# Kernel tuning notes

Hardware: AMD Instinct MI355X
Metric: run time of the kernel (lower is better)

Reference implementation:

```python
import jax, jax.numpy as jnp
import numpy as np
from jax import lax

D_MODEL = 128   # n_channels
OUT_C   = 128   # out_channels
D_STATE = 16
EXPAND  = 2
D_INNER = EXPAND * D_MODEL  # 256
D_CONV  = 4
DT_RANK = (D_MODEL + 15) // 16  # 8
LN_EPS  = 1e-5


def setup_inputs() -> dict:
    key = jax.random.key(0)
    ks = jax.random.split(key, 8)
    s = lambda k, shape: jax.random.normal(k, shape, jnp.float32) * 0.02
    return {
        "x1": jax.random.normal(ks[0], (2, D_MODEL, 64, 64), jnp.float32),
        "W_in": s(ks[1], (D_MODEL, 2 * D_INNER)),              # in_proj (no bias)
        "conv_w": s(ks[2], (D_INNER, 1, D_CONV)),              # depthwise conv kernel (O, I/g, K)
        "conv_b": jnp.zeros((D_INNER,), jnp.float32),
        "W_x": s(ks[3], (D_INNER, DT_RANK + 2 * D_STATE)),     # x_proj (no bias)
        "W_dt": s(ks[4], (DT_RANK, D_INNER)),                  # dt_proj
        "b_dt": s(ks[5], (D_INNER,)),
        "A_log": jnp.log(jnp.broadcast_to(
            jnp.arange(1, D_STATE + 1, dtype=jnp.float32), (D_INNER, D_STATE))),
        "D": jnp.ones((D_INNER,), jnp.float32),
        "W_out": s(ks[6], (D_INNER, OUT_C)),                   # out_proj (no bias)
        "ln_g": jnp.ones((OUT_C,), jnp.float32),
        "ln_b": jnp.zeros((OUT_C,), jnp.float32),
    }


def _mamba(x, W_in, conv_w, conv_b, W_x, W_dt, b_dt, A_log, D, W_out):
    # x: (b, L, d_model)
    b, L, _ = x.shape
    xz = x @ W_in                               # (b, L, 2*d_inner)
    xin, z = jnp.split(xz, 2, axis=-1)
    # causal depthwise conv1d over L
    xp = jnp.pad(xin, ((0, 0), (D_CONV - 1, 0), (0, 0)))
    xc = lax.conv_general_dilated(
        xp, conv_w, window_strides=(1,), padding='VALID',
        dimension_numbers=('NLC', 'OIL', 'NLC'),
        feature_group_count=D_INNER)
    xc = jax.nn.silu(xc + conv_b)               # (b, L, d_inner)
    # input-dependent SSM params
    xdbl = xc @ W_x                             # (b, L, dt_rank + 2*d_state)
    dt, Bm, Cm = jnp.split(xdbl, [DT_RANK, DT_RANK + D_STATE], axis=-1)
    dt = jax.nn.softplus(dt @ W_dt + b_dt)      # (b, L, d_inner)
    A = -jnp.exp(A_log)                         # (d_inner, d_state)
    dA = jnp.exp(dt[..., None] * A)                             # (b, L, d_inner, d_state)
    dBu = dt[..., None] * Bm[:, :, None, :] * xc[..., None]     # (b, L, d_inner, d_state)

    def step(h, inp):
        dA_t, dBu_t, C_t = inp                  # (b,d,s), (b,d,s), (b,s)
        h = dA_t * h + dBu_t
        y = jnp.einsum('bds,bs->bd', h, C_t)
        return h, y

    h0 = jnp.zeros((b, D_INNER, D_STATE), xc.dtype)
    _, ys = lax.scan(step, h0, (dA.transpose(1, 0, 2, 3),
                                dBu.transpose(1, 0, 2, 3),
                                Cm.transpose(1, 0, 2)))
    y = ys.transpose(1, 0, 2) + xc * D          # (b, L, d_inner)
    y = y * jax.nn.silu(z)                      # gated
    return y @ W_out                            # (b, L, out_c)


def reference(x1, W_in, conv_w, conv_b, W_x, W_dt, b_dt, A_log, D, W_out, ln_g, ln_b):
    b, c, h, w = x1.shape
    x = x1.transpose(0, 2, 3, 1).reshape(b, h * w, c)
    y = _mamba(x, W_in, conv_w, conv_b, W_x, W_dt, b_dt, A_log, D, W_out)
    mu = y.mean(-1, keepdims=True)
    var = ((y - mu) ** 2).mean(-1, keepdims=True)
    y = (y - mu) * lax.rsqrt(var + LN_EPS) * ln_g + ln_b
    return y.reshape(b, h, w, OUT_C).transpose(0, 3, 1, 2)
```

## Files before the change

kernel.cpp:

```cpp
#include <hip/hip_runtime.h>
#include <math.h>

#define B_ 2
#define DMODEL 128
#define DIN 256
#define DSTATE 16
#define DTR 8
#define OUTC 128
#define Lseq 4096
#define NC 256
#define LC 16

__device__ __forceinline__ float siluf(float x){ return x / (1.f + __expf(-x)); }

__device__ __forceinline__ void build_dA(float e1, float* dAv){
    float e2 = e1*e1, e4 = e2*e2, e8 = e4*e4;
    dAv[0]=e1;         dAv[1]=e2;         dAv[2]=e2*e1;       dAv[3]=e4;
    dAv[4]=e4*e1;      dAv[5]=e4*e2;      dAv[6]=e4*dAv[2];   dAv[7]=e8;
    dAv[8]=e8*e1;      dAv[9]=e8*e2;      dAv[10]=e8*dAv[2];  dAv[11]=e8*e4;
    dAv[12]=e8*dAv[4]; dAv[13]=e8*dAv[5]; dAv[14]=e8*dAv[6];  dAv[15]=e8*e8;
}

__device__ __forceinline__ float softplusf(float a){
    return (a > 20.f) ? a : __logf(1.f + __expf(a));
}

__global__ __launch_bounds__(256) void k_inconv_scan1(const float* __restrict__ x1,
        const float* __restrict__ Win,
        const float* __restrict__ convw, const float* __restrict__ convb,
        const float* __restrict__ Wx, const float* __restrict__ Wdt,
        const float* __restrict__ bdt, const float* __restrict__ Alog,
        float* __restrict__ zs, float* __restrict__ xc, float* __restrict__ dt,
        float* __restrict__ Bm, float* __restrict__ Cm, float2* __restrict__ PSw){
    __shared__ float sbuf[10240];
    __shared__ float xcs[16*257];
    __shared__ float xdbl[16*40];
    float* xt  = sbuf;
    float* Wxs = sbuf;
    int blk = blockIdx.x;
    int b  = blk >> 8;
    int cb = blk & 255;
    int l0 = cb << 4;
    int t  = threadIdx.x;

    const float* xb = x1 + (size_t)b * DMODEL * Lseq;
    for (int e = t; e < 128*19; e += 256){
        int c = e / 19, p = e - c*19;
        int l = l0 - 3 + p;
        xt[c*20 + p] = (l >= 0) ? xb[(size_t)c*Lseq + l] : 0.f;
    }
    __syncthreads();

    float acc0[19], acc1[16];
    #pragma unroll
    for (int p=0;p<19;++p){acc0[p]=0.f;}
    #pragma unroll
    for (int p=0;p<16;++p){acc1[p]=0.f;}
    #pragma unroll 4
    for (int k=0;k<DMODEL;++k){
        float w0 = Win[k*512 + t];
        float w1 = Win[k*512 + t + 256];
        const float4* xp = (const float4*)&xt[k*20];
        float4 v0 = xp[0], v1 = xp[1], v2 = xp[2], v3 = xp[3], v4 = xp[4];
        float xv[19] = { v0.x,v0.y,v0.z,v0.w, v1.x,v1.y,v1.z,v1.w,
                         v2.x,v2.y,v2.z,v2.w, v3.x,v3.y,v3.z,v3.w,
                         v4.x,v4.y,v4.z };
        #pragma unroll
        for (int p=0;p<19;++p) acc0[p] = fmaf(xv[p], w0, acc0[p]);
        #pragma unroll
        for (int p=0;p<16;++p) acc1[p] = fmaf(xv[p+3], w1, acc1[p]);
    }
    {
        float* zp = zs + ((size_t)(b*Lseq + l0))*DIN + t;
        #pragma unroll
        for (int p=0;p<16;++p) zp[p*DIN] = siluf(acc1[p]);
    }

    {
        float cw0 = convw[t*4+0], cw1 = convw[t*4+1], cw2 = convw[t*4+2], cw3 = convw[t*4+3];
        float bb = convb[t];
        float* xcg = xc + ((size_t)(b*Lseq + l0))*DIN + t;
        #pragma unroll
        for (int l = 0; l < 16; ++l){
            float acc = bb;
            acc = fmaf(acc0[l],   cw0, acc);
            acc = fmaf(acc0[l+1], cw1, acc);
            acc = fmaf(acc0[l+2], cw2, acc);
            acc = fmaf(acc0[l+3], cw3, acc);
            float v = siluf(acc);
            xcs[l*257 + t] = v;
            xcg[l*DIN] = v;
        }
    }
    __syncthreads();

    {
        const float4* Wg = (const float4*)Wx;
        float4* Ws = (float4*)Wxs;
        #pragma unroll
        for (int e = t; e < 2560; e += 256)
            Ws[e] = Wg[e];
    }
    __syncthreads();

    if (t < 128){
        int jg = t & 7;
        int lg = t >> 3;
        int j0 = jg * 5;
        float a0=0.f, a1=0.f, a2=0.f, a3=0.f, a4=0.f;
        const float* xrow = xcs + lg*257;
        const float* wbase = Wxs + j0;
        #pragma unroll 8
        for (int d = 0; d < 256; ++d){
            float xv = xrow[d];
            const float* wr = wbase + d*40;
            a0 = fmaf(xv, wr[0], a0);
            a1 = fmaf(xv, wr[1], a1);
            a2 = fmaf(xv, wr[2], a2);
            a3 = fmaf(xv, wr[3], a3);
            a4 = fmaf(xv, wr[4], a4);
        }
        float* xo = xdbl + lg*40 + j0;
        xo[0]=a0; xo[1]=a1; xo[2]=a2; xo[3]=a3; xo[4]=a4;
    }
    __syncthreads();

    {
        float wd[DTR];
        #pragma unroll
        for (int r=0;r<DTR;++r) wd[r] = Wdt[r*DIN + t];
        float bv = bdt[t];
        float Av[16];
        {
            const float4* Ap = (const float4*)(Alog + t*DSTATE);
            #pragma unroll
            for (int q=0;q<4;++q){
                float4 a = Ap[q];
                Av[q*4]   = -__expf(a.x);
                Av[q*4+1] = -__expf(a.y);
                Av[q*4+2] = -__expf(a.z);
                Av[q*4+3] = -__expf(a.w);
            }
        }
        bool fastA = true;
        #pragma unroll
        for (int i=1;i<16;++i)
            fastA = fastA && (fabsf(Av[i] - (float)(i+1)*Av[0]) <= 1e-6f*fabsf(Av[i]));
        float P[16], S[16];
        #pragma unroll
        for (int s=0;s<16;++s){ P[s]=1.f; S[s]=0.f; }
        float* dtg = dt + ((size_t)(b*Lseq + l0))*DIN + t;
        #pragma unroll 4
        for (int l=0;l<16;++l){
            float a = bv;
            #pragma unroll
            for (int r=0;r<DTR;++r) a = fmaf(xdbl[l*40 + r], wd[r], a);
            float dtv = softplusf(a);
            dtg[l*DIN] = dtv;
            float xcv = xcs[l*257 + t];
            float dx  = dtv*xcv;
            const float4* Bv = (const float4*)&xdbl[l*40 + DTR];
            float4 B0 = Bv[0], B1 = Bv[1], B2 = Bv[2], B3 = Bv[3];
            float dAv[16];
            if (fastA){
                build_dA(__expf(dtv*Av[0]), dAv);
            } else {
                #pragma unroll
                for (int i=0;i<16;++i) dAv[i] = __expf(dtv*Av[i]);
            }
            #define ST1(i, bval) { P[i] *= dAv[i]; S[i] = fmaf(dAv[i], S[i], dx*(bval)); }
            ST1(0,B0.x) ST1(1,B0.y) ST1(2,B0.z) ST1(3,B0.w)
            ST1(4,B1.x) ST1(5,B1.y) ST1(6,B1.z) ST1(7,B1.w)
            ST1(8,B2.x) ST1(9,B2.y) ST1(10,B2.z) ST1(11,B2.w)
            ST1(12,B3.x) ST1(13,B3.y) ST1(14,B3.z) ST1(15,B3.w)
            #undef ST1
        }
        float2* ps2 = PSw + ((size_t)(b*NC + cb))*4096;
        #pragma unroll
        for (int s=0;s<16;++s) ps2[s*256 + t] = make_float2(P[s], S[s]);
    }
    for (int o = t; o < 512; o += 256){
        int l = o >> 5, q = o & 31;
        float v = xdbl[l*40 + DTR + q];
        size_t g = ((size_t)(b*Lseq + l0 + l))*DSTATE;
        if (q < DSTATE) Bm[g + q] = v;
        else            Cm[g + (q - DSTATE)] = v;
    }
}

__global__ __launch_bounds__(256) void k_scan2(const float2* __restrict__ PSw,
        float* __restrict__ Iw){
    __shared__ float2 gps[16][16];
    __shared__ float  ge [16][16];
    int blk = blockIdx.x;
    int b  = blk >> 8;
    int r0 = (blk & 255) * 16;
    int t  = threadIdx.x;
    int rr = t & 15;
    int cg = t >> 4;
    size_t base = ((size_t)(b*NC + cg*16))*4096 + r0 + rr;
    float Pl[16], Sl[16];
    float Pa = 1.f, Sa = 0.f;
    #pragma unroll
    for (int i=0;i<16;++i){
        float2 ps = PSw[base + (size_t)i*4096];
        Pl[i] = ps.x; Sl[i] = ps.y;
        Pa = ps.x * Pa;
        Sa = fmaf(ps.x, Sa, ps.y);
    }
    gps[cg][rr] = make_float2(Pa, Sa);
    __syncthreads();
    if (t < 16){
        float H = 0.f;
        #pragma unroll
        for (int g=0; g<16; ++g){
            float2 ps = gps[g][t];
            ge[g][t] = H;
            H = fmaf(ps.x, H, ps.y);
        }
    }
    __syncthreads();
    float H = ge[cg][rr];
    #pragma unroll
    for (int i=0;i<16;++i){
        Iw[base + (size_t)i*4096] = H;
        H = fmaf(Pl[i], H, Sl[i]);
    }
}

__global__ __launch_bounds__(256) void k_scan3out(const float* __restrict__ dt,
        const float* __restrict__ xc, const float* __restrict__ zs,
        const float* __restrict__ Bm, const float* __restrict__ Cm,
        const float* __restrict__ Alog, const float* __restrict__ Dv,
        const float* __restrict__ Iw,
        const float* __restrict__ Wout, const float* __restrict__ lng,
        const float* __restrict__ lnb, float* __restrict__ out){
    __shared__ float ysm[256*18];
    __shared__ float os[128*18];
    __shared__ float Bs[LC*DSTATE];
    __shared__ float Cs[LC*DSTATE];
    int blk = blockIdx.x;
    int b = blk >> 8, c = blk & 255;
    int l0 = c * LC;
    int t = threadIdx.x;
    size_t gb = (size_t)(b*Lseq + l0);
    Bs[t] = Bm[gb*DSTATE + t];
    Cs[t] = Cm[gb*DSTATE + t];
    float Av[16];
    {
        const float4* Ap = (const float4*)(Alog + t*DSTATE);
        #pragma unroll
        for (int q=0;q<4;++q){
            float4 a = Ap[q];
            Av[q*4]   = -__expf(a.x);
            Av[q*4+1] = -__expf(a.y);
            Av[q*4+2] = -__expf(a.z);
            Av[q*4+3] = -__expf(a.w);
        }
    }
    bool fastA = true;
    #pragma unroll
    for (int i=1;i<16;++i)
        fastA = fastA && (fabsf(Av[i] - (float)(i+1)*Av[0]) <= 1e-6f*fabsf(Av[i]));
    float h[16];
    {
        const float* Ip = Iw + ((size_t)(b*NC + c))*4096 + t;
        #pragma unroll
        for (int s=0;s<16;++s) h[s] = Ip[s*256];
    }
    float Dd = Dv[t];
    float dtv[LC], xcv[LC], zvv[LC];
    {
        const float* dtp = dt + gb*DIN + t;
        const float* xcp = xc + gb*DIN + t;
        const float* zsp = zs + gb*DIN + t;
        #pragma unroll
        for (int l=0;l<LC;++l){
            dtv[l] = dtp[l*DIN];
            xcv[l] = xcp[l*DIN];
            zvv[l] = zsp[l*DIN];
        }
    }
    __syncthreads();
    #pragma unroll
    for (int l=0;l<LC;++l){
        float dtl = dtv[l];
        float dx  = dtl*xcv[l];
        const float4* Bv = (const float4*)&Bs[l*DSTATE];
        const float4* Cv = (const float4*)&Cs[l*DSTATE];
        float4 B0 = Bv[0], B1 = Bv[1], B2 = Bv[2], B3 = Bv[3];
        float4 C0 = Cv[0], C1 = Cv[1], C2 = Cv[2], C3 = Cv[3];
        float dAv[16];
        if (fastA){
            build_dA(__expf(dtl*Av[0]), dAv);
        } else {
            #pragma unroll
            for (int i=0;i<16;++i) dAv[i] = __expf(dtl*Av[i]);
        }
        float y = 0.f;
        #define ST3(i, bval, cval) { h[i] = fmaf(dAv[i], h[i], dx*(bval)); y = fmaf(h[i], (cval), y); }
        ST3(0,B0.x,C0.x) ST3(1,B0.y,C0.y) ST3(2,B0.z,C0.z) ST3(3,B0.w,C0.w)
        ST3(4,B1.x,C1.x) ST3(5,B1.y,C1.y) ST3(6,B1.z,C1.z) ST3(7,B1.w,C1.w)
        ST3(8,B2.x,C2.x) ST3(9,B2.y,C2.y) ST3(10,B2.z,C2.z) ST3(11,B2.w,C2.w)
        ST3(12,B3.x,C3.x) ST3(13,B3.y,C3.y) ST3(14,B3.z,C3.z) ST3(15,B3.w,C3.w)
        #undef ST3
        ysm[t*18 + l] = (y + Dd*xcv[l])*zvv[l];
    }
    __syncthreads();
    int lg = t >> 5, cg = t & 31;
    int l0t = lg*2, c0 = cg*4;
    float acc[2][4];
    #pragma unroll
    for (int i=0;i<2;++i)
        #pragma unroll
        for (int j=0;j<4;++j) acc[i][j]=0.f;
    #pragma unroll 4
    for (int k=0;k<DIN;++k){
        float2 yv = *(const float2*)&ysm[k*18 + l0t];
        float4 wv = *(const float4*)&Wout[k*OUTC + c0];
        acc[0][0]=fmaf(yv.x,wv.x,acc[0][0]); acc[0][1]=fmaf(yv.x,wv.y,acc[0][1]);
        acc[0][2]=fmaf(yv.x,wv.z,acc[0][2]); acc[0][3]=fmaf(yv.x,wv.w,acc[0][3]);
        acc[1][0]=fmaf(yv.y,wv.x,acc[1][0]); acc[1][1]=fmaf(yv.y,wv.y,acc[1][1]);
        acc[1][2]=fmaf(yv.y,wv.z,acc[1][2]); acc[1][3]=fmaf(yv.y,wv.w,acc[1][3]);
    }
    float4 gm = *(const float4*)&lng[c0];
    float4 bt = *(const float4*)&lnb[c0];
    #pragma unroll
    for (int i=0;i<2;++i){
        float rs = acc[i][0]+acc[i][1]+acc[i][2]+acc[i][3];
        #pragma unroll
        for (int m=16;m>0;m>>=1) rs += __shfl_xor(rs, m, 64);
        float mu = rs * (1.f/128.f);
        float d0 = acc[i][0]-mu, d1 = acc[i][1]-mu, d2 = acc[i][2]-mu, d3 = acc[i][3]-mu;
        float sq = d0*d0+d1*d1+d2*d2+d3*d3;
        #pragma unroll
        for (int m=16;m>0;m>>=1) sq += __shfl_xor(sq, m, 64);
        float rstd = rsqrtf(sq * (1.f/128.f) + 1e-5f);
        int lidx = l0t + i;
        os[(c0+0)*18 + lidx] = d0*rstd*gm.x + bt.x;
        os[(c0+1)*18 + lidx] = d1*rstd*gm.y + bt.y;
        os[(c0+2)*18 + lidx] = d2*rstd*gm.z + bt.z;
        os[(c0+3)*18 + lidx] = d3*rstd*gm.w + bt.w;
    }
    __syncthreads();
    {
        int cc = t >> 1, sel = t & 1;
        const float* ip = &os[cc*18 + sel*8];
        float2 a0 = *(const float2*)(ip);
        float2 a1 = *(const float2*)(ip+2);
        float2 a2 = *(const float2*)(ip+4);
        float2 a3 = *(const float2*)(ip+6);
        float* op = out + ((size_t)(b*OUTC + cc))*Lseq + l0 + sel*8;
        *(float4*)(op)   = make_float4(a0.x,a0.y,a1.x,a1.y);
        *(float4*)(op+4) = make_float4(a2.x,a2.y,a3.x,a3.y);
    }
}

extern "C" void kernel_launch(void* const* d_in, const int* in_sizes, int n_in,
                              void* d_out, int out_size, void* d_ws, size_t ws_size,
                              hipStream_t stream) {
    const float* x1    = (const float*)d_in[0];
    const float* Win   = (const float*)d_in[1];
    const float* convw = (const float*)d_in[2];
    const float* convb = (const float*)d_in[3];
    const float* Wx    = (const float*)d_in[4];
    const float* Wdt   = (const float*)d_in[5];
    const float* bdt   = (const float*)d_in[6];
    const float* Alog  = (const float*)d_in[7];
    const float* Dv    = (const float*)d_in[8];
    const float* Wout  = (const float*)d_in[9];
    const float* lng   = (const float*)d_in[10];
    const float* lnb   = (const float*)d_in[11];
    float* out = (float*)d_out;

    float* ws  = (float*)d_ws;
    float* Iw  = ws;
    float* zs  = Iw  + 2097152;
    float* xc  = zs  + 2097152;
    float* dt  = xc  + 2097152;
    float* Bm  = dt  + 2097152;
    float* Cm  = Bm  + 131072;
    float2* PSw = (float2*)(Cm + 131072);

    k_inconv_scan1<<<512, 256, 0, stream>>>(x1, Win, convw, convb, Wx, Wdt, bdt, Alog,
                                            zs, xc, dt, Bm, Cm, PSw);
    k_scan2       <<<512, 256, 0, stream>>>(PSw, Iw);
    k_scan3out    <<<512, 256, 0, stream>>>(dt, xc, zs, Bm, Cm, Alog, Dv, Iw,
                                            Wout, lng, lnb, out);
}
```

Before: 157.3 us.

## Fuse three kernels into one persistent kernel with software grid barriers

Merges the in-proj/conv/chunk-scan, the inter-chunk scan, and the output scan/out-proj/layernorm kernels into one kernel. Two atomic-counter grid barriers separate the phases. Per-chunk intermediates (z, xc, dt, B, C) now stay in registers and shared memory instead of round-tripping through global memory, which removes several MB of traffic and two launches. The barrier needs all 512 blocks resident at once; launch_bounds(256,2) is meant to ensure that, and the design adds spin-wait overhead plus a memset launch.

```diff
diff --git a/kernel.cpp b/kernel.cpp
--- a/kernel.cpp
+++ b/kernel.cpp
@@ -10,6 +10,7 @@
 #define Lseq 4096
 #define NC 256
 #define LC 16
+#define NBLK 512
 
 __device__ __forceinline__ float siluf(float x){ return x / (1.f + __expf(-x)); }
 
@@ -25,24 +26,39 @@
     return (a > 20.f) ? a : __logf(1.f + __expf(a));
 }
 
-__global__ __launch_bounds__(256) void k_inconv_scan1(const float* __restrict__ x1,
+__device__ __forceinline__ void gridbar(unsigned* cnt, int t){
+    __syncthreads();
+    if (t == 0){
+        __threadfence();
+        unsigned ticket = atomicAdd(cnt, 1u);
+        unsigned target = ((ticket >> 9) + 1u) << 9;
+        while (atomicAdd(cnt, 0u) < target){ __builtin_amdgcn_s_sleep(8); }
+        __threadfence();
+    }
+    __syncthreads();
+}
+
+__global__ __launch_bounds__(256, 2) void k_fused(const float* __restrict__ x1,
         const float* __restrict__ Win,
         const float* __restrict__ convw, const float* __restrict__ convb,
         const float* __restrict__ Wx, const float* __restrict__ Wdt,
         const float* __restrict__ bdt, const float* __restrict__ Alog,
-        float* __restrict__ zs, float* __restrict__ xc, float* __restrict__ dt,
-        float* __restrict__ Bm, float* __restrict__ Cm, float2* __restrict__ PSw){
+        const float* __restrict__ Dv, const float* __restrict__ Wout,
+        const float* __restrict__ lng, const float* __restrict__ lnb,
+        float2* __restrict__ PSw, float* __restrict__ Iw, unsigned* __restrict__ bar,
+        float* __restrict__ out){
     __shared__ float sbuf[10240];
     __shared__ float xcs[16*257];
     __shared__ float xdbl[16*40];
-    float* xt  = sbuf;
-    float* Wxs = sbuf;
+
     int blk = blockIdx.x;
     int b  = blk >> 8;
     int cb = blk & 255;
     int l0 = cb << 4;
     int t  = threadIdx.x;
 
+    float* xt  = sbuf;
+    float* Wxs = sbuf;
     const float* xb = x1 + (size_t)b * DMODEL * Lseq;
     for (int e = t; e < 128*19; e += 256){
         int c = e / 19, p = e - c*19;
@@ -70,16 +86,13 @@
         #pragma unroll
         for (int p=0;p<16;++p) acc1[p] = fmaf(xv[p+3], w1, acc1[p]);
     }
-    {
-        float* zp = zs + ((size_t)(b*Lseq + l0))*DIN + t;
-        #pragma unroll
-        for (int p=0;p<16;++p) zp[p*DIN] = siluf(acc1[p]);
-    }
+    float zvv[16];
+    #pragma unroll
+    for (int p=0;p<16;++p) zvv[p] = siluf(acc1[p]);
 
     {
         float cw0 = convw[t*4+0], cw1 = convw[t*4+1], cw2 = convw[t*4+2], cw3 = convw[t*4+3];
         float bb = convb[t];
-        float* xcg = xc + ((size_t)(b*Lseq + l0))*DIN + t;
         #pragma unroll
         for (int l = 0; l < 16; ++l){
             float acc = bb;
@@ -87,9 +100,7 @@
             acc = fmaf(acc0[l+1], cw1, acc);
             acc = fmaf(acc0[l+2], cw2, acc);
             acc = fmaf(acc0[l+3], cw3, acc);
-            float v = siluf(acc);
-            xcs[l*257 + t] = v;
-            xcg[l*DIN] = v;
+            xcs[l*257 + t] = siluf(acc);
         }
     }
     __syncthreads();
@@ -125,12 +136,13 @@
     }
     __syncthreads();
 
+    float Av[16], dtv[16];
+    bool fastA = true;
     {
         float wd[DTR];
         #pragma unroll
         for (int r=0;r<DTR;++r) wd[r] = Wdt[r*DIN + t];
         float bv = bdt[t];
-        float Av[16];
         {
             const float4* Ap = (const float4*)(Alog + t*DSTATE);
             #pragma unroll
@@ -142,31 +154,29 @@
                 Av[q*4+3] = -__expf(a.w);
             }
         }
-        bool fastA = true;
         #pragma unroll
         for (int i=1;i<16;++i)
             fastA = fastA && (fabsf(Av[i] - (float)(i+1)*Av[0]) <= 1e-6f*fabsf(Av[i]));
         float P[16], S[16];
         #pragma unroll
         for (int s=0;s<16;++s){ P[s]=1.f; S[s]=0.f; }
-        float* dtg = dt + ((size_t)(b*Lseq + l0))*DIN + t;
-        #pragma unroll 4
+        #pragma unroll
         for (int l=0;l<16;++l){
             float a = bv;
             #pragma unroll
             for (int r=0;r<DTR;++r) a = fmaf(xdbl[l*40 + r], wd[r], a);
-            float dtv = softplusf(a);
-            dtg[l*DIN] = dtv;
+            float dtvl = softplusf(a);
+            dtv[l] = dtvl;
             float xcv = xcs[l*257 + t];
-            float dx  = dtv*xcv;
+            float dx  = dtvl*xcv;
             const float4* Bv = (const float4*)&xdbl[l*40 + DTR];
             float4 B0 = Bv[0], B1 = Bv[1], B2 = Bv[2], B3 = Bv[3];
             float dAv[16];
             if (fastA){
-                build_dA(__expf(dtv*Av[0]), dAv);
+                build_dA(__expf(dtvl*Av[0]), dAv);
             } else {
                 #pragma unroll
-                for (int i=0;i<16;++i) dAv[i] = __expf(dtv*Av[i]);
+                for (int i=0;i<16;++i) dAv[i] = __expf(dtvl*Av[i]);
             }
             #define ST1(i, bval) { P[i] *= dAv[i]; S[i] = fmaf(dAv[i], S[i], dx*(bval)); }
             ST1(0,B0.x) ST1(1,B0.y) ST1(2,B0.z) ST1(3,B0.w)
@@ -179,116 +189,64 @@
         #pragma unroll
         for (int s=0;s<16;++s) ps2[s*256 + t] = make_float2(P[s], S[s]);
     }
-    for (int o = t; o < 512; o += 256){
-        int l = o >> 5, q = o & 31;
-        float v = xdbl[l*40 + DTR + q];
-        size_t g = ((size_t)(b*Lseq + l0 + l))*DSTATE;
-        if (q < DSTATE) Bm[g + q] = v;
-        else            Cm[g + (q - DSTATE)] = v;
-    }
-}
-
-__global__ __launch_bounds__(256) void k_scan2(const float2* __restrict__ PSw,
-        float* __restrict__ Iw){
-    __shared__ float2 gps[16][16];
-    __shared__ float  ge [16][16];
-    int blk = blockIdx.x;
-    int b  = blk >> 8;
-    int r0 = (blk & 255) * 16;
-    int t  = threadIdx.x;
-    int rr = t & 15;
-    int cg = t >> 4;
-    size_t base = ((size_t)(b*NC + cg*16))*4096 + r0 + rr;
-    float Pl[16], Sl[16];
-    float Pa = 1.f, Sa = 0.f;
-    #pragma unroll
-    for (int i=0;i<16;++i){
-        float2 ps = PSw[base + (size_t)i*4096];
-        Pl[i] = ps.x; Sl[i] = ps.y;
-        Pa = ps.x * Pa;
-        Sa = fmaf(ps.x, Sa, ps.y);
-    }
-    gps[cg][rr] = make_float2(Pa, Sa);
-    __syncthreads();
-    if (t < 16){
-        float H = 0.f;
-        #pragma unroll
-        for (int g=0; g<16; ++g){
-            float2 ps = gps[g][t];
-            ge[g][t] = H;
-            H = fmaf(ps.x, H, ps.y);
-        }
-    }
-    __syncthreads();
-    float H = ge[cg][rr];
-    #pragma unroll
-    for (int i=0;i<16;++i){
-        Iw[base + (size_t)i*4096] = H;
-        H = fmaf(Pl[i], H, Sl[i]);
-    }
-}
-
-__global__ __launch_bounds__(256) void k_scan3out(const float* __restrict__ dt,
-        const float* __restrict__ xc, const float* __restrict__ zs,
-        const float* __restrict__ Bm, const float* __restrict__ Cm,
-        const float* __restrict__ Alog, const float* __restrict__ Dv,
-        const float* __restrict__ Iw,
-        const float* __restrict__ Wout, const float* __restrict__ lng,
-        const float* __restrict__ lnb, float* __restrict__ out){
-    __shared__ float ysm[256*18];
-    __shared__ float os[128*18];
-    __shared__ float Bs[LC*DSTATE];
-    __shared__ float Cs[LC*DSTATE];
-    int blk = blockIdx.x;
-    int b = blk >> 8, c = blk & 255;
-    int l0 = c * LC;
-    int t = threadIdx.x;
-    size_t gb = (size_t)(b*Lseq + l0);
-    Bs[t] = Bm[gb*DSTATE + t];
-    Cs[t] = Cm[gb*DSTATE + t];
-    float Av[16];
-    {
-        const float4* Ap = (const float4*)(Alog + t*DSTATE);
-        #pragma unroll
-        for (int q=0;q<4;++q){
-            float4 a = Ap[q];
-            Av[q*4]   = -__expf(a.x);
-            Av[q*4+1] = -__expf(a.y);
-            Av[q*4+2] = -__expf(a.z);
-            Av[q*4+3] = -__expf(a.w);
-        }
-    }
-    bool fastA = true;
-    #pragma unroll
-    for (int i=1;i<16;++i)
-        fastA = fastA && (fabsf(Av[i] - (float)(i+1)*Av[0]) <= 1e-6f*fabsf(Av[i]));
+
+    gridbar(bar, t);
+
+    {
+        float2* gps = (float2*)sbuf;
+        float*  ge  = sbuf + 512;
+        int r0 = (blk & 255) * 16;
+        int rr = t & 15;
+        int cg2 = t >> 4;
+        size_t base = ((size_t)(b*NC + cg2*16))*4096 + r0 + rr;
+        float Pl[16], Sl[16];
+        float Pa = 1.f, Sa = 0.f;
+        #pragma unroll
+        for (int i=0;i<16;++i){
+            float2 ps = PSw[base + (size_t)i*4096];
+            Pl[i] = ps.x; Sl[i] = ps.y;
+            Pa = ps.x * Pa;
+            Sa = fmaf(ps.x, Sa, ps.y);
+        }
+        gps[cg2*16 + rr] = make_float2(Pa, Sa);
+        __syncthreads();
+        if (t < 16){
+            float H = 0.f;
+            #pragma unroll
+            for (int g=0; g<16; ++g){
+                float2 ps = gps[g*16 + t];
+                ge[g*16 + t] = H;
+                H = fmaf(ps.x, H, ps.y);
+            }
+        }
+        __syncthreads();
+        float H = ge[cg2*16 + rr];
+        #pragma unroll
+        for (int i=0;i<16;++i){
+            Iw[base + (size_t)i*4096] = H;
+            H = fmaf(Pl[i], H, Sl[i]);
+        }
+    }
+
+    gridbar(bar, t);
+
+    float* ysm = sbuf;
+    float* os  = sbuf + 4608;
     float h[16];
     {
-        const float* Ip = Iw + ((size_t)(b*NC + c))*4096 + t;
+        const float* Ip = Iw + ((size_t)(b*NC + cb))*4096 + t;
         #pragma unroll
         for (int s=0;s<16;++s) h[s] = Ip[s*256];
     }
     float Dd = Dv[t];
-    float dtv[LC], xcv[LC], zvv[LC];
-    {
-        const float* dtp = dt + gb*DIN + t;
-        const float* xcp = xc + gb*DIN + t;
-        const float* zsp = zs + gb*DIN + t;
-        #pragma unroll
-        for (int l=0;l<LC;++l){
-            dtv[l] = dtp[l*DIN];
-            xcv[l] = xcp[l*DIN];
-            zvv[l] = zsp[l*DIN];
-        }
-    }
-    __syncthreads();
     #pragma unroll
     for (int l=0;l<LC;++l){
         float dtl = dtv[l];
-        float dx  = dtl*xcv[l];
-        const float4* Bv = (const float4*)&Bs[l*DSTATE];
-        const float4* Cv = (const float4*)&Cs[l*DSTATE];
+        float xcv = xcs[l*257 + t];
+        float dx  = dtl*xcv;
+        const float4* Bv = (const float4*)&xdbl[l*40 + DTR];
         float4 B0 = Bv[0], B1 = Bv[1], B2 = Bv[2], B3 = Bv[3];
+        const float4* Cv = (const float4*)&xdbl[l*40 + DTR + DSTATE];
         float4 C0 = Cv[0], C1 = Cv[1], C2 = Cv[2], C3 = Cv[3];
         float dAv[16];
         if (fastA){
@@ -304,43 +262,45 @@
         ST3(8,B2.x,C2.x) ST3(9,B2.y,C2.y) ST3(10,B2.z,C2.z) ST3(11,B2.w,C2.w)
         ST3(12,B3.x,C3.x) ST3(13,B3.y,C3.y) ST3(14,B3.z,C3.z) ST3(15,B3.w,C3.w)
         #undef ST3
-        ysm[t*18 + l] = (y + Dd*xcv[l])*zvv[l];
-    }
-    __syncthreads();
-    int lg = t >> 5, cg = t & 31;
-    int l0t = lg*2, c0 = cg*4;
-    float acc[2][4];
-    #pragma unroll
-    for (int i=0;i<2;++i)
-        #pragma unroll
-        for (int j=0;j<4;++j) acc[i][j]=0.f;
-    #pragma unroll 4
-    for (int k=0;k<DIN;++k){
-        float2 yv = *(const float2*)&ysm[k*18 + l0t];
-        float4 wv = *(const float4*)&Wout[k*OUTC + c0];
-        acc[0][0]=fmaf(yv.x,wv.x,acc[0][0]); acc[0][1]=fmaf(yv.x,wv.y,acc[0][1]);
-        acc[0][2]=fmaf(yv.x,wv.z,acc[0][2]); acc[0][3]=fmaf(yv.x,wv.w,acc[0][3]);
-        acc[1][0]=fmaf(yv.y,wv.x,acc[1][0]); acc[1][1]=fmaf(yv.y,wv.y,acc[1][1]);
-        acc[1][2]=fmaf(yv.y,wv.z,acc[1][2]); acc[1][3]=fmaf(yv.y,wv.w,acc[1][3]);
-    }
-    float4 gm = *(const float4*)&lng[c0];
-    float4 bt = *(const float4*)&lnb[c0];
-    #pragma unroll
-    for (int i=0;i<2;++i){
-        float rs = acc[i][0]+acc[i][1]+acc[i][2]+acc[i][3];
-        #pragma unroll
-        for (int m=16;m>0;m>>=1) rs += __shfl_xor(rs, m, 64);
-        float mu = rs * (1.f/128.f);
-        float d0 = acc[i][0]-mu, d1 = acc[i][1]-mu, d2 = acc[i][2]-mu, d3 = acc[i][3]-mu;
-        float sq = d0*d0+d1*d1+d2*d2+d3*d3;
-        #pragma unroll
-        for (int m=16;m>0;m>>=1) sq += __shfl_xor(sq, m, 64);
-        float rstd = rsqrtf(sq * (1.f/128.f) + 1e-5f);
-        int lidx = l0t + i;
-        os[(c0+0)*18 + lidx] = d0*rstd*gm.x + bt.x;
-        os[(c0+1)*18 + lidx] = d1*rstd*gm.y + bt.y;
-        os[(c0+2)*18 + lidx] = d2*rstd*gm.z + bt.z;
-        os[(c0+3)*18 + lidx] = d3*rstd*gm.w + bt.w;
+        ysm[t*18 + l] = (y + Dd*xcv)*zvv[l];
+    }
+    __syncthreads();
+    {
+        int lg = t >> 5, cgc = t & 31;
+        int l0t = lg*2, c0 = cgc*4;
+        float acc[2][4];
+        #pragma unroll
+        for (int i=0;i<2;++i)
+            #pragma unroll
+            for (int j=0;j<4;++j) acc[i][j]=0.f;
+        #pragma unroll 4
+        for (int k=0;k<DIN;++k){
+            float2 yv = *(const float2*)&ysm[k*18 + l0t];
+            float4 wv = *(const float4*)&Wout[k*OUTC + c0];
+            acc[0][0]=fmaf(yv.x,wv.x,acc[0][0]); acc[0][1]=fmaf(yv.x,wv.y,acc[0][1]);
+            acc[0][2]=fmaf(yv.x,wv.z,acc[0][2]); acc[0][3]=fmaf(yv.x,wv.w,acc[0][3]);
+            acc[1][0]=fmaf(yv.y,wv.x,acc[1][0]); acc[1][1]=fmaf(yv.y,wv.y,acc[1][1]);
+            acc[1][2]=fmaf(yv.y,wv.z,acc[1][2]); acc[1][3]=fmaf(yv.y,wv.w,acc[1][3]);
+        }
+        float4 gm = *(const float4*)&lng[c0];
+        float4 bt = *(const float4*)&lnb[c0];
+        #pragma unroll
+        for (int i=0;i<2;++i){
+            float rs = acc[i][0]+acc[i][1]+acc[i][2]+acc[i][3];
+            #pragma unroll
+            for (int m=16;m>0;m>>=1) rs += __shfl_xor(rs, m, 64);
+            float mu = rs * (1.f/128.f);
+            float d0 = acc[i][0]-mu, d1 = acc[i][1]-mu, d2 = acc[i][2]-mu, d3 = acc[i][3]-mu;
+            float sq = d0*d0+d1*d1+d2*d2+d3*d3;
+            #pragma unroll
+            for (int m=16;m>0;m>>=1) sq += __shfl_xor(sq, m, 64);
+            float rstd = rsqrtf(sq * (1.f/128.f) + 1e-5f);
+            int lidx = l0t + i;
+            os[(c0+0)*18 + lidx] = d0*rstd*gm.x + bt.x;
+            os[(c0+1)*18 + lidx] = d1*rstd*gm.y + bt.y;
+            os[(c0+2)*18 + lidx] = d2*rstd*gm.z + bt.z;
+            os[(c0+3)*18 + lidx] = d3*rstd*gm.w + bt.w;
+        }
     }
     __syncthreads();
     {
@@ -373,18 +333,11 @@
     const float* lnb   = (const float*)d_in[11];
     float* out = (float*)d_out;
 
-    float* ws  = (float*)d_ws;
-    float* Iw  = ws;
-    float* zs  = Iw  + 2097152;
-    float* xc  = zs  + 2097152;
-    float* dt  = xc  + 2097152;
-    float* Bm  = dt  + 2097152;
-    float* Cm  = Bm  + 131072;
-    float2* PSw = (float2*)(Cm + 131072);
-
-    k_inconv_scan1<<<512, 256, 0, stream>>>(x1, Win, convw, convb, Wx, Wdt, bdt, Alog,
-                                            zs, xc, dt, Bm, Cm, PSw);
-    k_scan2       <<<512, 256, 0, stream>>>(PSw, Iw);
-    k_scan3out    <<<512, 256, 0, stream>>>(dt, xc, zs, Bm, Cm, Alog, Dv, Iw,
-                                            Wout, lng, lnb, out);
-}
+    float2*   PSw = (float2*)d_ws;
+    float*    Iw  = (float*)(PSw + 2097152);
+    unsigned* bar = (unsigned*)(Iw + 2097152);
+
+    hipMemsetAsync(bar, 0, 8, stream);
+    k_fused<<<512, 256, 0, stream>>>(x1, Win, convw, convb, Wx, Wdt, bdt, Alog,
+                                     Dv, Wout, lng, lnb, PSw, Iw, bar, out);
+}
```

After: 406.8 us. 2.59x slower.
